# Kernel optimization log

Hardware: AMD Instinct MI355X
Metric: run time of the kernel (lower is better)

Reference implementation:

```python
import jax, jax.numpy as jnp
import numpy as np

# Static config (Swin-T stage 1, SW-MSA)
B = 32; H = 56; W = 56; C = 96; NH = 3; WS = 7; SHIFT = 3
N = WS * WS                 # tokens per window (49)
NW = (H // WS) * (W // WS)  # windows per image (64)
HD = C // NH                # head dim (32)
SCALE = HD ** -0.5
EPS = 1e-3  # keras LayerNormalization default epsilon


def _rel_index():
    # Matches tf.stack(tf.meshgrid(h, w)) with default 'xy' indexing
    xx, yy = np.meshgrid(np.arange(WS), np.arange(WS))
    coords = np.stack([xx, yy]).reshape(2, -1)              # [2, 49]
    rel = (coords[:, :, None] - coords[:, None, :]).transpose(1, 2, 0)
    rel[:, :, 0] += WS - 1
    rel[:, :, 1] += WS - 1
    rel[:, :, 0] *= 2 * WS - 1
    return rel.sum(-1)                                       # [49, 49]

REL_IDX = jnp.asarray(_rel_index())


def _attn_mask():
    # Standard Swin shifted-window attention mask
    img = np.zeros((H, W))
    cnt = 0
    sl = (slice(0, -WS), slice(-WS, -SHIFT), slice(-SHIFT, None))
    for hs in sl:
        for ws_ in sl:
            img[hs, ws_] = cnt
            cnt += 1
    win = img.reshape(H // WS, WS, W // WS, WS).transpose(0, 2, 1, 3).reshape(-1, N)
    diff = win[:, None, :] - win[:, :, None]
    return jnp.asarray(np.where(diff != 0, -100.0, 0.0), dtype=np.float32)  # [nW,49,49]

MASK = _attn_mask()


def _ln(x, g, b):
    mu = x.mean(-1, keepdims=True)
    var = ((x - mu) ** 2).mean(-1, keepdims=True)
    return (x - mu) / jnp.sqrt(var + EPS) * g + b


def setup_inputs() -> dict:
    key = jax.random.key(0)
    ks = jax.random.split(key, 6)
    f32 = jnp.float32
    return {
        "x": jax.random.normal(ks[0], (B, H * W, C), f32),
        "norm1_g": jnp.ones((C,), f32), "norm1_b": jnp.zeros((C,), f32),
        "qkv_w": jax.random.normal(ks[1], (C, 3 * C), f32) * 0.02,
        "qkv_b": jnp.zeros((3 * C,), f32),
        "bias_table": jax.random.normal(ks[2], ((2 * WS - 1) ** 2, NH), f32) * 0.02,
        "proj_w": jax.random.normal(ks[3], (C, C), f32) * 0.02,
        "proj_b": jnp.zeros((C,), f32),
        "norm2_g": jnp.ones((C,), f32), "norm2_b": jnp.zeros((C,), f32),
        "fc1_w": jax.random.normal(ks[4], (C, 4 * C), f32) * 0.02,
        "fc1_b": jnp.zeros((4 * C,), f32),
        "fc2_w": jax.random.normal(ks[5], (4 * C, C), f32) * 0.02,
        "fc2_b": jnp.zeros((C,), f32),
    }


def reference(x, norm1_g, norm1_b, qkv_w, qkv_b, bias_table, proj_w, proj_b,
              norm2_g, norm2_b, fc1_w, fc1_b, fc2_w, fc2_b):
    shortcut = x
    h = _ln(x, norm1_g, norm1_b).reshape(B, H, W, C)
    # cyclic shift (SW-MSA)
    h = jnp.roll(h, (-SHIFT, -SHIFT), axis=(1, 2))
    # window partition -> [B*nW, N, C]
    h = h.reshape(B, H // WS, WS, W // WS, WS, C).transpose(0, 1, 3, 2, 4, 5).reshape(-1, N, C)
    qkv = (h @ qkv_w + qkv_b).reshape(-1, N, 3, NH, HD).transpose(2, 0, 3, 1, 4)
    q, k, v = qkv[0], qkv[1], qkv[2]            # each [B*nW, NH, N, HD]
    attn = jnp.einsum('bhnd,bhmd->bhnm', q * SCALE, k)
    bias = bias_table[REL_IDX.reshape(-1)].reshape(N, N, NH).transpose(2, 0, 1)
    attn = attn + bias[None]
    attn = attn.reshape(B, NW, NH, N, N) + MASK[None, :, None]
    attn = attn.reshape(-1, NH, N, N)
    # NOTE: source applies softmax twice (once in branch, once unconditionally)
    attn = jax.nn.softmax(jax.nn.softmax(attn, axis=-1), axis=-1)
    o = jnp.einsum('bhnm,bhmd->bhnd', attn, v).transpose(0, 2, 1, 3).reshape(-1, N, C)
    o = o @ proj_w + proj_b
    # window reverse + reverse cyclic shift
    o = o.reshape(B, H // WS, W // WS, WS, WS, C).transpose(0, 1, 3, 2, 4, 5).reshape(B, H, W, C)
    o = jnp.roll(o, (SHIFT, SHIFT), axis=(1, 2)).reshape(B, H * W, C)
    x = shortcut + o
    y = _ln(x, norm2_g, norm2_b)
    # NOTE: source Mlp applies gelu in Dense activation AND again in call -> double gelu
    y = jax.nn.gelu(y @ fc1_w + fc1_b, approximate=False)
    y = jax.nn.gelu(y, approximate=False)
    y = y @ fc2_w + fc2_b
    return x + y
```

## Files before the change

kernel.cpp:

```cpp
#include <hip/hip_runtime.h>
#include <math.h>

#define BB   32
#define HH   56
#define WWI  56
#define CC   96
#define NHD  3
#define WSZ  7
#define SHF  3
#define NTK  49
#define NWIN 64
#define HDM  32
#define TOT  (BB*HH*WWI)
#define QKSCALE 0.17677669529663687f
#define LEPS 1e-3f

typedef __attribute__((ext_vector_type(8))) short s8v;
typedef __attribute__((ext_vector_type(4))) float fx4;
typedef unsigned long long ull_t;

#define MFMA16(a,b,c) __builtin_amdgcn_mfma_f32_16x16x32_bf16((a),(b),(c),0,0,0)

__device__ __forceinline__ unsigned short f2bf(float f) {
    union { float f; unsigned u; } v; v.f = f;
    unsigned r = v.u + 0x7FFFu + ((v.u >> 16) & 1u);
    return (unsigned short)(r >> 16);
}

__device__ __forceinline__ float gelu_t(float x) {
    float x2 = x * x;
#if __has_builtin(__builtin_amdgcn_exp2f)
    float z = x * fmaf(-0.10294326f, x2, -2.3022082f);
    float e = __builtin_amdgcn_exp2f(z);
#else
    float z = x * fmaf(-0.07135529f, x2, -1.5957691f);
    float e = __expf(z);
#endif
    return x * __builtin_amdgcn_rcpf(1.f + e);
}

__device__ __forceinline__ int wtok_to_orig(int wt) {
    int win = wt / NTK;
    int p   = wt - win * NTK;
    int b   = win >> 6;
    int w   = win & 63;
    int wi = w >> 3, wj = w & 7;
    int pi = p / WSZ, pj = p - pi * WSZ;
    int r = wi * WSZ + pi + SHF; if (r >= HH) r -= HH;
    int c = wj * WSZ + pj + SHF; if (c >= WWI) c -= WWI;
    return b * (HH * WWI) + r * WWI + c;
}

__device__ __forceinline__ void ln_frag(const float* __restrict__ row,
                                        const float* __restrict__ gg,
                                        const float* __restrict__ bb,
                                        int g4, s8v ha[3])
{
    float h[24];
    #pragma unroll
    for (int ks = 0; ks < 3; ++ks) {
        fx4 v0 = *reinterpret_cast<const fx4*>(row + ks * 32 + g4 * 8);
        fx4 v1 = *reinterpret_cast<const fx4*>(row + ks * 32 + g4 * 8 + 4);
        h[ks*8+0]=v0.x; h[ks*8+1]=v0.y; h[ks*8+2]=v0.z; h[ks*8+3]=v0.w;
        h[ks*8+4]=v1.x; h[ks*8+5]=v1.y; h[ks*8+6]=v1.z; h[ks*8+7]=v1.w;
    }
    float s = 0.f, s2 = 0.f;
    #pragma unroll
    for (int j = 0; j < 24; ++j) { s += h[j]; s2 = fmaf(h[j], h[j], s2); }
    s  += __shfl_xor(s, 16);  s  += __shfl_xor(s, 32);
    s2 += __shfl_xor(s2, 16); s2 += __shfl_xor(s2, 32);
    const float mu = s * (1.f/CC);
    const float rs = rsqrtf(s2 * (1.f/CC) - mu * mu + LEPS);
    #pragma unroll
    for (int ks = 0; ks < 3; ++ks) {
        union { s8v v; unsigned short u[8]; } p;
        #pragma unroll
        for (int j = 0; j < 8; ++j) {
            int c = ks * 32 + g4 * 8 + j;
            p.u[j] = f2bf((h[ks*8+j] - mu) * rs * gg[c] + bb[c]);
        }
        ha[ks] = p.v;
    }
}

extern "C" __global__ void p0_prep(const float* __restrict__ qw, const float* __restrict__ pw,
                                   const float* __restrict__ w1, const float* __restrict__ w2,
                                   const float* __restrict__ btab,
                                   unsigned short* __restrict__ wsw)
{
    int i = blockIdx.x * 256 + threadIdx.x;
    if (i < 27648) {
        int e = i & 7, f = i >> 3;
        int lane = f & 63, fid = f >> 6;
        int ks = fid % 3, t = fid / 3;
        int nt = t % 6, ck = t / 6;
        int n = ck * 96 + nt * 16 + (lane & 15);
        int k = ks * 32 + (lane >> 4) * 8 + e;
        float v = qw[k * 288 + n];
        if (n < 96) v *= QKSCALE;
        wsw[i] = f2bf(v);
    } else if (i < 36864) {
        int j = i - 27648;
        int e = j & 7, f = j >> 3;
        int lane = f & 63, fid = f >> 6;
        int ks = fid % 3, nt = fid / 3;
        int n = nt * 16 + (lane & 15);
        int k = ks * 32 + (lane >> 4) * 8 + e;
        wsw[i] = f2bf(pw[k * 96 + n]);
    } else if (i < 73728) {
        int j = i - 36864;
        int e = j & 7, f = j >> 3;
        int lane = f & 63, fid = f >> 6;
        int ks = fid % 3, t = fid / 3;
        int nt = t & 3, ck = t >> 2;
        int n = ck * 64 + nt * 16 + (lane & 15);
        int k = ks * 32 + (lane >> 4) * 8 + e;
        wsw[i] = f2bf(w1[k * 384 + n]);
    } else if (i < 110592) {
        int j = i - 73728;
        int e = j & 7, f = j >> 3;
        int lane = f & 63, fid = f >> 6;
        int ks = fid & 1, t = fid >> 1;
        int nt = t % 6, ck = t / 6;
        int n = nt * 16 + (lane & 15);
        int k = ck * 64 + ks * 32 + (lane >> 4) * 8 + e;
        wsw[i] = f2bf(w2[k * 96 + n]);
    } else if (i < 159744) {
        float* bmf = (float*)(wsw + 110592);
        int j = i - 110592;
        int r = j & 3, lane = (j >> 2) & 63;
        int fid = j >> 8;
        int mtnt = fid & 15, t = fid >> 4;
        int mt = mtnt >> 2, nt = mtnt & 3;
        int hd = t % 3, cls = t / 3;
        int m = mt * 16 + (lane >> 4) * 4 + r; if (m > 48) m = 48;
        int n = nt * 16 + (lane & 15);
        float val = 0.f;
        if (n < 49) {
            int it = m / 7, jt = m - it * 7;
            int iu = n / 7, ju = n - iu * 7;
            int li  = (cls & 2) ? (it < 4 ? 1 : 2) : 0;
            int lj  = (cls & 1) ? (jt < 4 ? 1 : 2) : 0;
            int lui = (cls & 2) ? (iu < 4 ? 1 : 2) : 0;
            int luj = (cls & 1) ? (ju < 4 ? 1 : 2) : 0;
            int bidx = (jt - ju + 6) * 13 + (it - iu + 6);
            val = btab[bidx * 3 + hd] + ((li*3+lj) == (lui*3+luj) ? 0.f : -100.f);
        }
        bmf[j] = val;
    }
}

extern "C" __global__ void __launch_bounds__(256, 3) k1_qkv(
    const float* __restrict__ x, const float* __restrict__ g1, const float* __restrict__ b1,
    const unsigned short* __restrict__ qwtf, const float* __restrict__ qb,
    unsigned short* __restrict__ qkvb)
{
    const int tid = threadIdx.x, wave = tid >> 6, lane = tid & 63;
    const int l15 = lane & 15, g4 = lane >> 4;
    const int row0 = blockIdx.x * 64 + wave * 16;

    s8v ha[3];
    {
        const int orig = wtok_to_orig(row0 + l15);
        ln_frag(x + (size_t)orig * CC, g1, b1, g4, ha);
    }

    #pragma unroll
    for (int ck = 0; ck < 3; ++ck) {
        fx4 acc[6];
        #pragma unroll
        for (int nt = 0; nt < 6; ++nt) acc[nt] = (fx4){0.f,0.f,0.f,0.f};
        #pragma unroll
        for (int ks = 0; ks < 3; ++ks) {
            #pragma unroll
            for (int nt = 0; nt < 6; ++nt) {
                s8v b = *reinterpret_cast<const s8v*>(
                    &qwtf[(((ck * 6 + nt) * 3 + ks) * 64 + lane) * 8]);
                acc[nt] = MFMA16(ha[ks], b, acc[nt]);
            }
        }
        const int rowb = row0 + g4 * 4;
        const float qmul = (ck == 0) ? QKSCALE : 1.f;
        #pragma unroll
        for (int nt = 0; nt < 6; ++nt) {
            const int col = ck * 96 + nt * 16 + l15;
            const float qbc = qb[col] * qmul;
            #pragma unroll
            for (int r = 0; r < 4; ++r)
                qkvb[(size_t)(rowb + r) * 288 + col] = f2bf(acc[nt][r] + qbc);
        }
    }
}

extern "C" __global__ void __launch_bounds__(64, 3) k2_attn(
    unsigned short* __restrict__ qkvb, const float* __restrict__ bmf)
{
    __shared__ unsigned short P[64][72];
    const int lane = threadIdx.x;
    const int l15 = lane & 15, g4 = lane >> 4;
    const int task = blockIdx.x;
    const int win = task / 3, h = task - win * 3;
    const int g0  = win * NTK;
    const int w   = win & 63;
    const int cls = (((w >> 3) == 7) ? 2 : 0) + (((w & 7) == 7) ? 1 : 0);
    const float* BMF = bmf + (size_t)(cls * 3 + h) * 4096;

    s8v aq[4], bk[4];
    #pragma unroll
    for (int mt = 0; mt < 4; ++mt) {
        int tok = mt * 16 + l15; if (tok > 48) tok = 48;
        const unsigned short* qp = &qkvb[(size_t)(g0 + tok) * 288 + h * HDM + g4 * 8];
        aq[mt] = *reinterpret_cast<const s8v*>(qp);
        bk[mt] = *reinterpret_cast<const s8v*>(qp + 96);
    }

    fx4 sc[4][4];
    #pragma unroll
    for (int mt = 0; mt < 4; ++mt)
        #pragma unroll
        for (int nt = 0; nt < 4; ++nt)
            sc[mt][nt] = MFMA16(aq[mt], bk[nt], ((fx4){0.f,0.f,0.f,0.f}));

    #pragma unroll
    for (int mt = 0; mt < 4; ++mt) {
        fx4 bmv[4];
        #pragma unroll
        for (int nt = 0; nt < 4; ++nt)
            bmv[nt] = *reinterpret_cast<const fx4*>(&BMF[((mt * 4 + nt) << 8) + lane * 4]);
        #pragma unroll
        for (int r = 0; r < 4; ++r) {
            float rs1 = 0.f;
            #pragma unroll
            for (int nt = 0; nt < 4; ++nt) {
                const int n = nt * 16 + l15;
                float s = sc[mt][nt][r] + bmv[nt][r];
                float e = (n < NTK) ? __expf(s) : 0.f;
                sc[mt][nt][r] = e;
                rs1 += e;
            }
            rs1 += __shfl_xor(rs1, 1); rs1 += __shfl_xor(rs1, 2);
            rs1 += __shfl_xor(rs1, 4); rs1 += __shfl_xor(rs1, 8);
            const float iv1 = 1.f / rs1;
            float rs2 = 0.f;
            #pragma unroll
            for (int nt = 0; nt < 4; ++nt) {
                const int n = nt * 16 + l15;
                float e2 = (n < NTK) ? __expf(sc[mt][nt][r] * iv1) : 0.f;
                sc[mt][nt][r] = e2;
                rs2 += e2;
            }
            rs2 += __shfl_xor(rs2, 1); rs2 += __shfl_xor(rs2, 2);
            rs2 += __shfl_xor(rs2, 4); rs2 += __shfl_xor(rs2, 8);
            const float iv2 = 1.f / rs2;
            const int m = mt * 16 + g4 * 4 + r;
            #pragma unroll
            for (int nt = 0; nt < 4; ++nt)
                P[m][nt * 16 + l15] = f2bf(sc[mt][nt][r] * iv2);
        }
    }
    __syncthreads();

    fx4 oc[4][2];
    #pragma unroll
    for (int mt = 0; mt < 4; ++mt) { oc[mt][0] = (fx4){0.f,0.f,0.f,0.f}; oc[mt][1] = (fx4){0.f,0.f,0.f,0.f}; }
    #pragma unroll
    for (int ks = 0; ks < 2; ++ks) {
        s8v vb[2];
        #pragma unroll
        for (int nt = 0; nt < 2; ++nt) {
            union { s8v v; unsigned short u[8]; } pv;
            #pragma unroll
            for (int j = 0; j < 8; ++j) {
                int tok = ks * 32 + g4 * 8 + j; if (tok > 48) tok = 48;
                pv.u[j] = qkvb[(size_t)(g0 + tok) * 288 + 192 + h * HDM + nt * 16 + l15];
            }
            vb[nt] = pv.v;
        }
        #pragma unroll
        for (int mt = 0; mt < 4; ++mt) {
            s8v pa = *reinterpret_cast<const s8v*>(&P[mt * 16 + l15][ks * 32 + g4 * 8]);
            oc[mt][0] = MFMA16(pa, vb[0], oc[mt][0]);
            oc[mt][1] = MFMA16(pa, vb[1], oc[mt][1]);
        }
    }
    #pragma unroll
    for (int mt = 0; mt < 4; ++mt) {
        #pragma unroll
        for (int r = 0; r < 4; ++r) {
            const int m = mt * 16 + g4 * 4 + r;
            if (m < NTK) {
                qkvb[(size_t)(g0 + m) * 288 + h * HDM + l15]      = f2bf(oc[mt][0][r]);
                qkvb[(size_t)(g0 + m) * 288 + h * HDM + 16 + l15] = f2bf(oc[mt][1][r]);
            }
        }
    }
}

#define LDA 72
#define LDX2 100
extern "C" __global__ void __launch_bounds__(256, 3) k23_fused(
    const unsigned short* __restrict__ qkvb, const unsigned short* __restrict__ pwtf,
    const float* __restrict__ pb, const float* __restrict__ x,
    const float* __restrict__ g2, const float* __restrict__ b2,
    const unsigned short* __restrict__ w1f, const float* __restrict__ bf1,
    const unsigned short* __restrict__ w2f, const float* __restrict__ bf2,
    float* __restrict__ out)
{
    __shared__ float X2[64][LDX2];
    __shared__ unsigned short Ac[64 * LDA];
    const int tid = threadIdx.x, wave = tid >> 6, lane = tid & 63;
    const int l15 = lane & 15, g4 = lane >> 4;
    const int row0 = blockIdx.x * 64 + wave * 16;

    s8v a[3];
    {
        const int t = row0 + l15;
        const int b = t / (HH * WWI), rc = t - b * (HH * WWI);
        const int orr = rc / WWI, occ = rc - orr * WWI;
        int wr = orr + (HH - SHF); if (wr >= HH) wr -= HH;
        int wc = occ + (WWI - SHF); if (wc >= WWI) wc -= WWI;
        const int wtok = (b * 64 + (wr / WSZ) * 8 + (wc / WSZ)) * NTK
                         + (wr % WSZ) * WSZ + (wc % WSZ);
        const unsigned short* arow = qkvb + (size_t)wtok * 288 + g4 * 8;
        a[0] = *reinterpret_cast<const s8v*>(arow);
        a[1] = *reinterpret_cast<const s8v*>(arow + 32);
        a[2] = *reinterpret_cast<const s8v*>(arow + 64);
    }
    {
        fx4 acc[6];
        #pragma unroll
        for (int nt = 0; nt < 6; ++nt) acc[nt] = (fx4){0.f,0.f,0.f,0.f};
        #pragma unroll
        for (int ks = 0; ks < 3; ++ks) {
            #pragma unroll
            for (int nt = 0; nt < 6; ++nt) {
                s8v b = *reinterpret_cast<const s8v*>(&pwtf[((nt * 3 + ks) * 64 + lane) * 8]);
                acc[nt] = MFMA16(a[ks], b, acc[nt]);
            }
        }
        #pragma unroll
        for (int nt = 0; nt < 6; ++nt) {
            const int col = nt * 16 + l15;
            const float pbc = pb[col];
            #pragma unroll
            for (int r = 0; r < 4; ++r) {
                const int tr = row0 + g4 * 4 + r;
                X2[wave * 16 + g4 * 4 + r][col] = acc[nt][r] + pbc + x[(size_t)tr * CC + col];
            }
        }
    }

    s8v ha[3];
    ln_frag(&X2[wave * 16 + l15][0], g2, b2, g4, ha);

    fx4 oacc[6];
    #pragma unroll
    for (int nt = 0; nt < 6; ++nt) oacc[nt] = (fx4){0.f,0.f,0.f,0.f};

    #pragma unroll 1
    for (int ck = 0; ck < 6; ++ck) {
        fx4 a1[4];
        #pragma unroll
        for (int nt = 0; nt < 4; ++nt) a1[nt] = (fx4){0.f,0.f,0.f,0.f};
        #pragma unroll
        for (int ks = 0; ks < 3; ++ks) {
            #pragma unroll
            for (int nt = 0; nt < 4; ++nt) {
                s8v b = *reinterpret_cast<const s8v*>(
                    &w1f[(((ck * 4 + nt) * 3 + ks) * 64 + lane) * 8]);
                a1[nt] = MFMA16(ha[ks], b, a1[nt]);
            }
        }
        #pragma unroll
        for (int nt = 0; nt < 4; ++nt) {
            const float bb = bf1[ck * 64 + nt * 16 + l15];
            #pragma unroll
            for (int r = 0; r < 4; ++r) {
                float v0 = a1[nt][r] + bb;
                Ac[(wave*16 + g4*4 + r) * LDA + nt*16 + l15] = f2bf(gelu_t(gelu_t(v0)));
            }
        }
        #pragma unroll
        for (int ks = 0; ks < 2; ++ks) {
            s8v aa = *reinterpret_cast<const s8v*>(&Ac[(wave*16 + l15)*LDA + ks*32 + g4*8]);
            #pragma unroll
            for (int nt = 0; nt < 6; ++nt) {
                s8v b = *reinterpret_cast<const s8v*>(
                    &w2f[(((ck * 6 + nt) * 2 + ks) * 64 + lane) * 8]);
                oacc[nt] = MFMA16(aa, b, oacc[nt]);
            }
        }
    }

    const int rowb = row0 + g4 * 4;
    #pragma unroll
    for (int nt = 0; nt < 6; ++nt) {
        const int col = nt * 16 + l15;
        const float bb = bf2[col];
        #pragma unroll
        for (int r = 0; r < 4; ++r) {
            out[(size_t)(rowb + r) * CC + col] =
                X2[wave * 16 + g4 * 4 + r][col] + oacc[nt][r] + bb;
        }
    }
}

extern "C" void kernel_launch(void* const* d_in, const int* in_sizes, int n_in,
                              void* d_out, int out_size, void* d_ws, size_t ws_size,
                              hipStream_t stream)
{
    const float* x    = (const float*)d_in[0];
    const float* n1g  = (const float*)d_in[1];
    const float* n1b  = (const float*)d_in[2];
    const float* qw   = (const float*)d_in[3];
    const float* qb   = (const float*)d_in[4];
    const float* btab = (const float*)d_in[5];
    const float* pw   = (const float*)d_in[6];
    const float* pb   = (const float*)d_in[7];
    const float* n2g  = (const float*)d_in[8];
    const float* n2b  = (const float*)d_in[9];
    const float* w1   = (const float*)d_in[10];
    const float* bf1  = (const float*)d_in[11];
    const float* w2   = (const float*)d_in[12];
    const float* bf2  = (const float*)d_in[13];
    float* out = (float*)d_out;

    unsigned short* qkvb = (unsigned short*)d_ws;
    unsigned short* wbf  = qkvb + (size_t)TOT * 288;
    unsigned short* qwtf = wbf;
    unsigned short* pwtf = qwtf + 27648;
    unsigned short* w1f  = pwtf + 9216;
    unsigned short* w2f  = w1f + 36864;
    float* bmf = (float*)(wbf + 110592);

    p0_prep  <<<624, 256, 0, stream>>>(qw, pw, w1, w2, btab, wbf);
    k1_qkv   <<<TOT/64, 256, 0, stream>>>(x, n1g, n1b, qwtf, qb, qkvb);
    k2_attn  <<<BB*NWIN*NHD, 64, 0, stream>>>(qkvb, bmf);
    k23_fused<<<TOT/64, 256, 0, stream>>>(qkvb, pwtf, pb, x, n2g, n2b,
                                          w1f, bf1, w2f, bf2, out);
}
```

Before: 126.7 us.

## Fuse QKV projection with windowed attention, keeping Q/K in shared memory

Merges the QKV projection kernel and the attention kernel into one kernel that runs one block per window. Q and K stay in LDS, and only V goes to a compact 96-column global buffer, which the attention output then overwrites in place. This removes the full 288-column bf16 QKV round trip through global memory and one kernel launch. In exchange, 15 of the 64 padded rows per block are wasted in the projection, one wave sits idle during attention, occupancy drops to 2 blocks per SIMD because of the larger LDS use, and V is still re-read from global.

```diff
diff --git a/kernel.cpp b/kernel.cpp
--- a/kernel.cpp
+++ b/kernel.cpp
@@ -150,19 +150,25 @@
     }
 }
 
-extern "C" __global__ void __launch_bounds__(256, 3) k1_qkv(
+#define LDQ 104
+extern "C" __global__ void __launch_bounds__(256, 2) k12_fused(
     const float* __restrict__ x, const float* __restrict__ g1, const float* __restrict__ b1,
     const unsigned short* __restrict__ qwtf, const float* __restrict__ qb,
-    unsigned short* __restrict__ qkvb)
+    const float* __restrict__ bmf, unsigned short* __restrict__ ovb)
 {
+    __shared__ unsigned short Qs[64 * LDQ];
+    __shared__ unsigned short Ks[64 * LDQ];
+    __shared__ unsigned short P[3][64 * 72];
     const int tid = threadIdx.x, wave = tid >> 6, lane = tid & 63;
     const int l15 = lane & 15, g4 = lane >> 4;
-    const int row0 = blockIdx.x * 64 + wave * 16;
+    const int win = blockIdx.x;
+    const int g0  = win * NTK;
 
     s8v ha[3];
     {
-        const int orig = wtok_to_orig(row0 + l15);
-        ln_frag(x + (size_t)orig * CC, g1, b1, g4, ha);
+        int row = wave * 16 + l15;
+        int tok = row > 48 ? 48 : row;
+        ln_frag(x + (size_t)wtok_to_orig(g0 + tok) * CC, g1, b1, g4, ha);
     }
 
     #pragma unroll
@@ -179,118 +185,133 @@
                 acc[nt] = MFMA16(ha[ks], b, acc[nt]);
             }
         }
-        const int rowb = row0 + g4 * 4;
-        const float qmul = (ck == 0) ? QKSCALE : 1.f;
-        #pragma unroll
-        for (int nt = 0; nt < 6; ++nt) {
-            const int col = ck * 96 + nt * 16 + l15;
-            const float qbc = qb[col] * qmul;
-            #pragma unroll
-            for (int r = 0; r < 4; ++r)
-                qkvb[(size_t)(rowb + r) * 288 + col] = f2bf(acc[nt][r] + qbc);
-        }
-    }
-}
-
-extern "C" __global__ void __launch_bounds__(64, 3) k2_attn(
-    unsigned short* __restrict__ qkvb, const float* __restrict__ bmf)
-{
-    __shared__ unsigned short P[64][72];
-    const int lane = threadIdx.x;
-    const int l15 = lane & 15, g4 = lane >> 4;
-    const int task = blockIdx.x;
-    const int win = task / 3, h = task - win * 3;
-    const int g0  = win * NTK;
-    const int w   = win & 63;
-    const int cls = (((w >> 3) == 7) ? 2 : 0) + (((w & 7) == 7) ? 1 : 0);
-    const float* BMF = bmf + (size_t)(cls * 3 + h) * 4096;
-
-    s8v aq[4], bk[4];
-    #pragma unroll
-    for (int mt = 0; mt < 4; ++mt) {
-        int tok = mt * 16 + l15; if (tok > 48) tok = 48;
-        const unsigned short* qp = &qkvb[(size_t)(g0 + tok) * 288 + h * HDM + g4 * 8];
-        aq[mt] = *reinterpret_cast<const s8v*>(qp);
-        bk[mt] = *reinterpret_cast<const s8v*>(qp + 96);
-    }
-
-    fx4 sc[4][4];
-    #pragma unroll
-    for (int mt = 0; mt < 4; ++mt)
-        #pragma unroll
-        for (int nt = 0; nt < 4; ++nt)
-            sc[mt][nt] = MFMA16(aq[mt], bk[nt], ((fx4){0.f,0.f,0.f,0.f}));
-
-    #pragma unroll
-    for (int mt = 0; mt < 4; ++mt) {
-        fx4 bmv[4];
-        #pragma unroll
-        for (int nt = 0; nt < 4; ++nt)
-            bmv[nt] = *reinterpret_cast<const fx4*>(&BMF[((mt * 4 + nt) << 8) + lane * 4]);
-        #pragma unroll
-        for (int r = 0; r < 4; ++r) {
-            float rs1 = 0.f;
-            #pragma unroll
-            for (int nt = 0; nt < 4; ++nt) {
-                const int n = nt * 16 + l15;
-                float s = sc[mt][nt][r] + bmv[nt][r];
-                float e = (n < NTK) ? __expf(s) : 0.f;
-                sc[mt][nt][r] = e;
-                rs1 += e;
-            }
-            rs1 += __shfl_xor(rs1, 1); rs1 += __shfl_xor(rs1, 2);
-            rs1 += __shfl_xor(rs1, 4); rs1 += __shfl_xor(rs1, 8);
-            const float iv1 = 1.f / rs1;
-            float rs2 = 0.f;
-            #pragma unroll
-            for (int nt = 0; nt < 4; ++nt) {
-                const int n = nt * 16 + l15;
-                float e2 = (n < NTK) ? __expf(sc[mt][nt][r] * iv1) : 0.f;
-                sc[mt][nt][r] = e2;
-                rs2 += e2;
-            }
-            rs2 += __shfl_xor(rs2, 1); rs2 += __shfl_xor(rs2, 2);
-            rs2 += __shfl_xor(rs2, 4); rs2 += __shfl_xor(rs2, 8);
-            const float iv2 = 1.f / rs2;
-            const int m = mt * 16 + g4 * 4 + r;
+        const int rowb = wave * 16 + g4 * 4;
+        if (ck == 0) {
+            #pragma unroll
+            for (int nt = 0; nt < 6; ++nt) {
+                const int col = nt * 16 + l15;
+                const float qbc = qb[col] * QKSCALE;
+                #pragma unroll
+                for (int r = 0; r < 4; ++r)
+                    Qs[(rowb + r) * LDQ + col] = f2bf(acc[nt][r] + qbc);
+            }
+        } else if (ck == 1) {
+            #pragma unroll
+            for (int nt = 0; nt < 6; ++nt) {
+                const int col = nt * 16 + l15;
+                const float qbc = qb[96 + col];
+                #pragma unroll
+                for (int r = 0; r < 4; ++r)
+                    Ks[(rowb + r) * LDQ + col] = f2bf(acc[nt][r] + qbc);
+            }
+        } else {
+            #pragma unroll
+            for (int nt = 0; nt < 6; ++nt) {
+                const int col = nt * 16 + l15;
+                const float qbc = qb[192 + col];
+                #pragma unroll
+                for (int r = 0; r < 4; ++r) {
+                    const int rr = rowb + r;
+                    if (rr < NTK)
+                        ovb[(size_t)(g0 + rr) * 96 + col] = f2bf(acc[nt][r] + qbc);
+                }
+            }
+        }
+    }
+    __syncthreads();
+
+    if (wave < 3) {
+        const int h = wave;
+        const int w = win & 63;
+        const int cls = (((w >> 3) == 7) ? 2 : 0) + (((w & 7) == 7) ? 1 : 0);
+        const float* BMF = bmf + (size_t)(cls * 3 + h) * 4096;
+        unsigned short* Ph = &P[h][0];
+
+        s8v aq[4], bk[4];
+        #pragma unroll
+        for (int mt = 0; mt < 4; ++mt) {
+            const int rm = mt * 16 + l15;
+            aq[mt] = *reinterpret_cast<const s8v*>(&Qs[rm * LDQ + h * 32 + g4 * 8]);
+            bk[mt] = *reinterpret_cast<const s8v*>(&Ks[rm * LDQ + h * 32 + g4 * 8]);
+        }
+
+        fx4 sc[4][4];
+        #pragma unroll
+        for (int mt = 0; mt < 4; ++mt)
             #pragma unroll
             for (int nt = 0; nt < 4; ++nt)
-                P[m][nt * 16 + l15] = f2bf(sc[mt][nt][r] * iv2);
-        }
-    }
-    __syncthreads();
-
-    fx4 oc[4][2];
-    #pragma unroll
-    for (int mt = 0; mt < 4; ++mt) { oc[mt][0] = (fx4){0.f,0.f,0.f,0.f}; oc[mt][1] = (fx4){0.f,0.f,0.f,0.f}; }
-    #pragma unroll
-    for (int ks = 0; ks < 2; ++ks) {
-        s8v vb[2];
-        #pragma unroll
-        for (int nt = 0; nt < 2; ++nt) {
-            union { s8v v; unsigned short u[8]; } pv;
-            #pragma unroll
-            for (int j = 0; j < 8; ++j) {
-                int tok = ks * 32 + g4 * 8 + j; if (tok > 48) tok = 48;
-                pv.u[j] = qkvb[(size_t)(g0 + tok) * 288 + 192 + h * HDM + nt * 16 + l15];
-            }
-            vb[nt] = pv.v;
-        }
+                sc[mt][nt] = MFMA16(aq[mt], bk[nt], ((fx4){0.f,0.f,0.f,0.f}));
+
         #pragma unroll
         for (int mt = 0; mt < 4; ++mt) {
-            s8v pa = *reinterpret_cast<const s8v*>(&P[mt * 16 + l15][ks * 32 + g4 * 8]);
-            oc[mt][0] = MFMA16(pa, vb[0], oc[mt][0]);
-            oc[mt][1] = MFMA16(pa, vb[1], oc[mt][1]);
-        }
-    }
-    #pragma unroll
-    for (int mt = 0; mt < 4; ++mt) {
-        #pragma unroll
-        for (int r = 0; r < 4; ++r) {
-            const int m = mt * 16 + g4 * 4 + r;
-            if (m < NTK) {
-                qkvb[(size_t)(g0 + m) * 288 + h * HDM + l15]      = f2bf(oc[mt][0][r]);
-                qkvb[(size_t)(g0 + m) * 288 + h * HDM + 16 + l15] = f2bf(oc[mt][1][r]);
+            fx4 bmv[4];
+            #pragma unroll
+            for (int nt = 0; nt < 4; ++nt)
+                bmv[nt] = *reinterpret_cast<const fx4*>(&BMF[((mt * 4 + nt) << 8) + lane * 4]);
+            #pragma unroll
+            for (int r = 0; r < 4; ++r) {
+                float rs1 = 0.f;
+                #pragma unroll
+                for (int nt = 0; nt < 4; ++nt) {
+                    const int n = nt * 16 + l15;
+                    float s = sc[mt][nt][r] + bmv[nt][r];
+                    float e = (n < NTK) ? __expf(s) : 0.f;
+                    sc[mt][nt][r] = e;
+                    rs1 += e;
+                }
+                rs1 += __shfl_xor(rs1, 1); rs1 += __shfl_xor(rs1, 2);
+                rs1 += __shfl_xor(rs1, 4); rs1 += __shfl_xor(rs1, 8);
+                const float iv1 = 1.f / rs1;
+                float rs2 = 0.f;
+                #pragma unroll
+                for (int nt = 0; nt < 4; ++nt) {
+                    const int n = nt * 16 + l15;
+                    float e2 = (n < NTK) ? __expf(sc[mt][nt][r] * iv1) : 0.f;
+                    sc[mt][nt][r] = e2;
+                    rs2 += e2;
+                }
+                rs2 += __shfl_xor(rs2, 1); rs2 += __shfl_xor(rs2, 2);
+                rs2 += __shfl_xor(rs2, 4); rs2 += __shfl_xor(rs2, 8);
+                const float iv2 = 1.f / rs2;
+                const int m = mt * 16 + g4 * 4 + r;
+                #pragma unroll
+                for (int nt = 0; nt < 4; ++nt)
+                    Ph[m * 72 + nt * 16 + l15] = f2bf(sc[mt][nt][r] * iv2);
+            }
+        }
+
+        fx4 oc[4][2];
+        #pragma unroll
+        for (int mt = 0; mt < 4; ++mt) { oc[mt][0] = (fx4){0.f,0.f,0.f,0.f}; oc[mt][1] = (fx4){0.f,0.f,0.f,0.f}; }
+        #pragma unroll
+        for (int ks = 0; ks < 2; ++ks) {
+            s8v vb[2];
+            #pragma unroll
+            for (int nt = 0; nt < 2; ++nt) {
+                union { s8v v; unsigned short u[8]; } pv;
+                #pragma unroll
+                for (int j = 0; j < 8; ++j) {
+                    int tok = ks * 32 + g4 * 8 + j; if (tok > 48) tok = 48;
+                    pv.u[j] = ovb[(size_t)(g0 + tok) * 96 + h * 32 + nt * 16 + l15];
+                }
+                vb[nt] = pv.v;
+            }
+            #pragma unroll
+            for (int mt = 0; mt < 4; ++mt) {
+                s8v pa = *reinterpret_cast<const s8v*>(&Ph[(mt * 16 + l15) * 72 + ks * 32 + g4 * 8]);
+                oc[mt][0] = MFMA16(pa, vb[0], oc[mt][0]);
+                oc[mt][1] = MFMA16(pa, vb[1], oc[mt][1]);
+            }
+        }
+        #pragma unroll
+        for (int mt = 0; mt < 4; ++mt) {
+            #pragma unroll
+            for (int r = 0; r < 4; ++r) {
+                const int m = mt * 16 + g4 * 4 + r;
+                if (m < NTK) {
+                    ovb[(size_t)(g0 + m) * 96 + h * 32 + l15]      = f2bf(oc[mt][0][r]);
+                    ovb[(size_t)(g0 + m) * 96 + h * 32 + 16 + l15] = f2bf(oc[mt][1][r]);
+                }
             }
         }
     }
@@ -299,7 +320,7 @@
 #define LDA 72
 #define LDX2 100
 extern "C" __global__ void __launch_bounds__(256, 3) k23_fused(
-    const unsigned short* __restrict__ qkvb, const unsigned short* __restrict__ pwtf,
+    const unsigned short* __restrict__ ovb, const unsigned short* __restrict__ pwtf,
     const float* __restrict__ pb, const float* __restrict__ x,
     const float* __restrict__ g2, const float* __restrict__ b2,
     const unsigned short* __restrict__ w1f, const float* __restrict__ bf1,
@@ -321,7 +342,7 @@
         int wc = occ + (WWI - SHF); if (wc >= WWI) wc -= WWI;
         const int wtok = (b * 64 + (wr / WSZ) * 8 + (wc / WSZ)) * NTK
                          + (wr % WSZ) * WSZ + (wc % WSZ);
-        const unsigned short* arow = qkvb + (size_t)wtok * 288 + g4 * 8;
+        const unsigned short* arow = ovb + (size_t)wtok * 96 + g4 * 8;
         a[0] = *reinterpret_cast<const s8v*>(arow);
         a[1] = *reinterpret_cast<const s8v*>(arow + 32);
         a[2] = *reinterpret_cast<const s8v*>(arow + 64);
@@ -425,8 +446,8 @@
     const float* bf2  = (const float*)d_in[13];
     float* out = (float*)d_out;
 
-    unsigned short* qkvb = (unsigned short*)d_ws;
-    unsigned short* wbf  = qkvb + (size_t)TOT * 288;
+    unsigned short* ovb  = (unsigned short*)d_ws;
+    unsigned short* wbf  = ovb + (size_t)TOT * 96;
     unsigned short* qwtf = wbf;
     unsigned short* pwtf = qwtf + 27648;
     unsigned short* w1f  = pwtf + 9216;
@@ -434,8 +455,7 @@
     float* bmf = (float*)(wbf + 110592);
 
     p0_prep  <<<624, 256, 0, stream>>>(qw, pw, w1, w2, btab, wbf);
-    k1_qkv   <<<TOT/64, 256, 0, stream>>>(x, n1g, n1b, qwtf, qb, qkvb);
-    k2_attn  <<<BB*NWIN*NHD, 64, 0, stream>>>(qkvb, bmf);
-    k23_fused<<<TOT/64, 256, 0, stream>>>(qkvb, pwtf, pb, x, n2g, n2b,
+    k12_fused<<<BB*NWIN, 256, 0, stream>>>(x, n1g, n1b, qwtf, qb, bmf, ovb);
+    k23_fused<<<TOT/64, 256, 0, stream>>>(ovb, pwtf, pb, x, n2g, n2b,
                                           w1f, bf1, w2f, bf2, out);
 }
```

Measured after the change: 121.2 us. 4.4% less time.
